# Kernel tuning notes

Hardware: AMD Instinct MI355X
Metric: run time of the kernel (lower is better)

Reference implementation:

```python
import jax, jax.numpy as jnp
import numpy as np
import math

B, S, D, H = 4, 2048, 1024, 16
DH = D // H  # per-head dim = 64
MASK_VAL = -1000000.0


def setup_inputs() -> dict:
    key = jax.random.key(0)
    ks = jax.random.split(key, 9)
    queries = jax.random.normal(ks[0], (B, S, D), dtype=jnp.float32)
    keys = jax.random.normal(ks[1], (B, S, D), dtype=jnp.float32)
    values = jax.random.normal(ks[2], (B, S, D), dtype=jnp.float32)
    valid_lens = jax.random.randint(ks[3], (B,), 0, S, dtype=jnp.int32)
    scale = 1.0 / math.sqrt(D)
    Wq = jax.random.normal(ks[4], (D, D), dtype=jnp.float32) * scale
    Wk = jax.random.normal(ks[5], (D, D), dtype=jnp.float32) * scale
    Wv = jax.random.normal(ks[6], (D, D), dtype=jnp.float32) * scale
    Wo = jax.random.normal(ks[7], (D, D), dtype=jnp.float32) * scale
    return {"queries": queries, "keys": keys, "values": values,
            "valid_lens": valid_lens, "Wq": Wq, "Wk": Wk, "Wv": Wv, "Wo": Wo}


def _split_heads(x):  # [B,S,D] -> [B,H,S,DH]
    b, s, _ = x.shape
    return x.reshape(b, s, H, DH).transpose(0, 2, 1, 3)


def reference(queries, keys, values, valid_lens, Wq, Wk, Wv, Wo):
    q = _split_heads(queries @ Wq)  # [B,H,S,DH]
    k = _split_heads(keys @ Wk)
    v = _split_heads(values @ Wv)
    scores = jnp.einsum('bhqd,bhkd->bhqk', q, k) / jnp.sqrt(jnp.float32(DH))
    # mask key positions >= valid_len[b] (sequence_mask with value=-1e6)
    key_pos = jnp.arange(S)  # [S]
    mask = key_pos[None, None, None, :] < valid_lens[:, None, None, None]  # [B,1,1,S]
    scores = jnp.where(mask, scores, MASK_VAL)
    attn = jax.nn.softmax(scores, axis=-1)  # [B,H,S,S] -- the 1GB intermediate
    out = jnp.einsum('bhqk,bhkd->bhqd', attn, v)  # [B,H,S,DH]
    out = out.transpose(0, 2, 1, 3).reshape(B, S, D)  # concat heads
    return out @ Wo
```

## Files before the change

kernel.cpp:

```cpp
#include <hip/hip_runtime.h>

#define BB 4
#define SS 2048
#define DD 1024
#define HH 16
#define DHH 64

typedef _Float16 half8 __attribute__((ext_vector_type(8)));
typedef _Float16 half4v __attribute__((ext_vector_type(4)));
typedef float floatx4 __attribute__((ext_vector_type(4)));

#define GLOBAL_AS __attribute__((address_space(1)))
#define LDS_AS __attribute__((address_space(3)))

__global__ void wt_kernel(const float* __restrict__ w0, const float* __restrict__ w1,
                          const float* __restrict__ w2, const float* __restrict__ w3,
                          _Float16* __restrict__ wt) {
  __shared__ float tile[32][33];
  int z = blockIdx.z;
  const float* w = (z == 0) ? w0 : (z == 1) ? w1 : (z == 2) ? w2 : w3;
  _Float16* dst = wt + (size_t)z * 1024 * 1024;
  int k0 = blockIdx.x * 32, n0 = blockIdx.y * 32;
  int tx = threadIdx.x & 31, ty = threadIdx.x >> 5;
#pragma unroll
  for (int r = ty; r < 32; r += 8) tile[r][tx] = w[(size_t)(k0 + r) * 1024 + n0 + tx];
  __syncthreads();
#pragma unroll
  for (int r = ty; r < 32; r += 8) dst[(size_t)(n0 + r) * 1024 + k0 + tx] = (_Float16)tile[tx][r];
}

__global__ void cvt3_kernel(const float* __restrict__ q, const float* __restrict__ k,
                            const float* __restrict__ v, _Float16* __restrict__ dst) {
  int z = blockIdx.y;
  const float* src = (z == 0) ? q : (z == 1) ? k : v;
  size_t i = ((size_t)blockIdx.x * 256 + threadIdx.x) * 8;
  float4 f0 = *(const float4*)(src + i);
  float4 f1 = *(const float4*)(src + i + 4);
  half8 h = {(_Float16)f0.x, (_Float16)f0.y, (_Float16)f0.z, (_Float16)f0.w,
             (_Float16)f1.x, (_Float16)f1.y, (_Float16)f1.z, (_Float16)f1.w};
  *(half8*)(dst + (size_t)z * 8388608 + i) = h;
}

__global__ __launch_bounds__(256) void qkv_gemm(const _Float16* __restrict__ Acat,
                                                const _Float16* __restrict__ Wt,
                                                _Float16* __restrict__ Qf,
                                                _Float16* __restrict__ Kf,
                                                _Float16* __restrict__ Vt) {
  __shared__ _Float16 lA[128 * 32];
  __shared__ _Float16 lB[128 * 32];
  int tid = threadIdx.x;
  int wave = tid >> 6, lane = tid & 63, quad = lane >> 4, l15 = lane & 15;
  int bn = blockIdx.x, bm = blockIdx.y;
  int proj = bm >> 6;
  int wm = wave >> 1, wn = wave & 1;

  const _Float16* A = Acat + (size_t)bm * 128 * 1024;
  const _Float16* W = Wt + (size_t)proj * 1024 * 1024;

  floatx4 fzero = {0.f, 0.f, 0.f, 0.f};
  floatx4 acc[4][4];
#pragma unroll
  for (int i = 0; i < 4; ++i)
#pragma unroll
    for (int j = 0; j < 4; ++j) acc[i][j] = fzero;

  int g0 = tid, g1 = 256 + tid;
  int row0 = g0 >> 2, gc0 = (g0 & 3) ^ ((row0 >> 1) & 3);
  int row1 = g1 >> 2, gc1 = (g1 & 3) ^ ((row1 >> 1) & 3);
  const _Float16* a0 = A + ((size_t)row0 * 1024 + gc0 * 8);
  const _Float16* a1 = A + ((size_t)row1 * 1024 + gc1 * 8);
  const _Float16* b0 = W + ((size_t)(bn * 128 + row0) * 1024 + gc0 * 8);
  const _Float16* b1 = W + ((size_t)(bn * 128 + row1) * 1024 + gc1 * 8);

  for (int k0 = 0; k0 < 1024; k0 += 32) {
    __builtin_amdgcn_global_load_lds((const GLOBAL_AS void*)(a0 + k0),
                                     (LDS_AS void*)(lA + g0 * 8), 16, 0, 0);
    __builtin_amdgcn_global_load_lds((const GLOBAL_AS void*)(a1 + k0),
                                     (LDS_AS void*)(lA + g1 * 8), 16, 0, 0);
    __builtin_amdgcn_global_load_lds((const GLOBAL_AS void*)(b0 + k0),
                                     (LDS_AS void*)(lB + g0 * 8), 16, 0, 0);
    __builtin_amdgcn_global_load_lds((const GLOBAL_AS void*)(b1 + k0),
                                     (LDS_AS void*)(lB + g1 * 8), 16, 0, 0);
    __syncthreads();

    half8 af[4], bf[4];
#pragma unroll
    for (int i = 0; i < 4; ++i) {
      int row = wm * 64 + i * 16 + l15;
      af[i] = *(const half8*)(lA + (row * 4 + (quad ^ ((row >> 1) & 3))) * 8);
    }
#pragma unroll
    for (int j = 0; j < 4; ++j) {
      int row = wn * 64 + j * 16 + l15;
      bf[j] = *(const half8*)(lB + (row * 4 + (quad ^ ((row >> 1) & 3))) * 8);
    }
#pragma unroll
    for (int i = 0; i < 4; ++i)
#pragma unroll
      for (int j = 0; j < 4; ++j)
        acc[i][j] = __builtin_amdgcn_mfma_f32_16x16x32_f16(af[i], bf[j], acc[i][j], 0, 0, 0);
    __syncthreads();
  }

  int rloc = (bm & 63) * 128;
#pragma unroll
  for (int i = 0; i < 4; ++i) {
#pragma unroll
    for (int j = 0; j < 4; ++j) {
      int rowb = rloc + wm * 64 + i * 16 + quad * 4;
      int col = bn * 128 + wn * 64 + j * 16 + l15;
      if (proj == 0) {
#pragma unroll
        for (int r = 0; r < 4; ++r)
          Qf[(size_t)(rowb + r) * 1024 + col] = (_Float16)(acc[i][j][r] * 0.125f);
      } else if (proj == 1) {
#pragma unroll
        for (int r = 0; r < 4; ++r)
          Kf[(size_t)(rowb + r) * 1024 + col] = (_Float16)acc[i][j][r];
      } else {
        int b = rowb >> 11, s = rowb & 2047;
        half4v pk = {(_Float16)acc[i][j][0], (_Float16)acc[i][j][1],
                     (_Float16)acc[i][j][2], (_Float16)acc[i][j][3]};
        *(half4v*)(Vt + (size_t)(b * 1024 + col) * 2048 + s) = pk;
      }
    }
  }
}

__global__ __launch_bounds__(256) void gemm_out(const _Float16* __restrict__ A,
                                                const _Float16* __restrict__ Wt,
                                                float* __restrict__ C) {
  __shared__ _Float16 lA[128 * 32];
  __shared__ _Float16 lB[128 * 32];
  int tid = threadIdx.x;
  int wave = tid >> 6, lane = tid & 63, quad = lane >> 4, l15 = lane & 15;
  int bn = blockIdx.x, bm = blockIdx.y;
  int wm = wave >> 1, wn = wave & 1;

  floatx4 fzero = {0.f, 0.f, 0.f, 0.f};
  floatx4 acc[4][4];
#pragma unroll
  for (int i = 0; i < 4; ++i)
#pragma unroll
    for (int j = 0; j < 4; ++j) acc[i][j] = fzero;

  int g0 = tid, g1 = 256 + tid;
  int row0 = g0 >> 2, gc0 = (g0 & 3) ^ ((row0 >> 1) & 3);
  int row1 = g1 >> 2, gc1 = (g1 & 3) ^ ((row1 >> 1) & 3);
  const _Float16* a0 = A + ((size_t)(bm * 128 + row0) * 1024 + gc0 * 8);
  const _Float16* a1 = A + ((size_t)(bm * 128 + row1) * 1024 + gc1 * 8);
  const _Float16* b0 = Wt + ((size_t)(bn * 128 + row0) * 1024 + gc0 * 8);
  const _Float16* b1 = Wt + ((size_t)(bn * 128 + row1) * 1024 + gc1 * 8);

  for (int k0 = 0; k0 < 1024; k0 += 32) {
    __builtin_amdgcn_global_load_lds((const GLOBAL_AS void*)(a0 + k0),
                                     (LDS_AS void*)(lA + g0 * 8), 16, 0, 0);
    __builtin_amdgcn_global_load_lds((const GLOBAL_AS void*)(a1 + k0),
                                     (LDS_AS void*)(lA + g1 * 8), 16, 0, 0);
    __builtin_amdgcn_global_load_lds((const GLOBAL_AS void*)(b0 + k0),
                                     (LDS_AS void*)(lB + g0 * 8), 16, 0, 0);
    __builtin_amdgcn_global_load_lds((const GLOBAL_AS void*)(b1 + k0),
                                     (LDS_AS void*)(lB + g1 * 8), 16, 0, 0);
    __syncthreads();

    half8 af[4], bf[4];
#pragma unroll
    for (int i = 0; i < 4; ++i) {
      int row = wm * 64 + i * 16 + l15;
      af[i] = *(const half8*)(lA + (row * 4 + (quad ^ ((row >> 1) & 3))) * 8);
    }
#pragma unroll
    for (int j = 0; j < 4; ++j) {
      int row = wn * 64 + j * 16 + l15;
      bf[j] = *(const half8*)(lB + (row * 4 + (quad ^ ((row >> 1) & 3))) * 8);
    }
#pragma unroll
    for (int i = 0; i < 4; ++i)
#pragma unroll
      for (int j = 0; j < 4; ++j)
        acc[i][j] = __builtin_amdgcn_mfma_f32_16x16x32_f16(af[i], bf[j], acc[i][j], 0, 0, 0);
    __syncthreads();
  }

#pragma unroll
  for (int i = 0; i < 4; ++i)
#pragma unroll
    for (int j = 0; j < 4; ++j) {
      int rowb = bm * 128 + wm * 64 + i * 16 + quad * 4;
      int col = bn * 128 + wn * 64 + j * 16 + l15;
#pragma unroll
      for (int r = 0; r < 4; ++r) C[(size_t)(rowb + r) * 1024 + col] = acc[i][j][r];
    }
}

__global__ __launch_bounds__(256) void attn_kernel(const _Float16* __restrict__ Q,
                                                   const _Float16* __restrict__ K,
                                                   const _Float16* __restrict__ Vt,
                                                   const int* __restrict__ vlens,
                                                   _Float16* __restrict__ O) {
  __shared__ _Float16 lK[64 * 64];
  __shared__ _Float16 lV[64 * 64];
  __shared__ _Float16 lP[4 * 16 * 64];

  int tid = threadIdx.x, wave = tid >> 6, lane = tid & 63, quad = lane >> 4, l15 = lane & 15;
  int bh = blockIdx.y, b = bh >> 4, h = bh & 15;
  int q0 = blockIdx.x * 64;
  int vlen = vlens[b];
  int nch = (vlen == 0) ? (SS / 64) : ((vlen + 63) >> 6);
  float mask_val = (vlen == 0) ? 0.0f : -1.0e6f;

  const _Float16* qb = Q + ((size_t)(b * SS + q0 + wave * 16 + l15) * DD + h * 64 + quad * 8);
  half8 qf0 = *(const half8*)qb;
  half8 qf1 = *(const half8*)(qb + 32);

  float l_part[4] = {0.f, 0.f, 0.f, 0.f};
  floatx4 fzero = {0.f, 0.f, 0.f, 0.f};
  floatx4 o[4];
#pragma unroll
  for (int j = 0; j < 4; ++j) o[j] = fzero;

  for (int kc = 0; kc < nch; ++kc) {
    int kb = kc * 64;
#pragma unroll
    for (int ss = tid; ss < 512; ss += 256) {
      int row = ss >> 3, gc = ss & 7;
      int sidx = (row * 8 + (gc ^ (row & 7))) * 8;
      *(half8*)(lK + sidx) =
          *(const half8*)(K + ((size_t)(b * SS + kb + row) * DD + h * 64 + gc * 8));
      *(half8*)(lV + sidx) =
          *(const half8*)(Vt + ((size_t)(b * DD + h * 64 + row) * SS + kb + gc * 8));
    }
    __syncthreads();

    floatx4 sacc[4];
#pragma unroll
    for (int j = 0; j < 4; ++j) sacc[j] = fzero;
#pragma unroll
    for (int ks = 0; ks < 2; ++ks) {
      half8 qf = ks ? qf1 : qf0;
#pragma unroll
      for (int j = 0; j < 4; ++j) {
        int row = j * 16 + l15, gc = ks * 4 + quad;
        half8 kf = *(const half8*)(lK + (row * 8 + (gc ^ (row & 7))) * 8);
        sacc[j] = __builtin_amdgcn_mfma_f32_16x16x32_f16(qf, kf, sacc[j], 0, 0, 0);
      }
    }

    bool clean = (kb + 64 <= vlen);
#pragma unroll
    for (int j = 0; j < 4; ++j) {
      int key = kb + j * 16 + l15;
      bool valid = clean | (key < vlen);
#pragma unroll
      for (int r = 0; r < 4; ++r) {
        float s = valid ? sacc[j][r] : mask_val;
        float p = __expf(s);
        l_part[r] += p;
        int row = quad * 4 + r, col = j * 16 + l15;
        int gc = col >> 3, off = col & 7;
        lP[wave * 1024 + row * 64 + (gc ^ (row & 7)) * 8 + off] = (_Float16)p;
      }
    }

#pragma unroll
    for (int ks = 0; ks < 2; ++ks) {
      int gc = ks * 4 + quad;
      half8 pf = *(const half8*)(lP + wave * 1024 + l15 * 64 + (gc ^ (l15 & 7)) * 8);
#pragma unroll
      for (int j = 0; j < 4; ++j) {
        int row = j * 16 + l15;
        half8 vf = *(const half8*)(lV + (row * 8 + (gc ^ (row & 7))) * 8);
        o[j] = __builtin_amdgcn_mfma_f32_16x16x32_f16(pf, vf, o[j], 0, 0, 0);
      }
    }
    __syncthreads();
  }

  float inv_l[4];
#pragma unroll
  for (int r = 0; r < 4; ++r) {
    float l = l_part[r];
#pragma unroll
    for (int off = 1; off < 16; off <<= 1) l += __shfl_xor(l, off);
    inv_l[r] = 1.0f / l;
  }
#pragma unroll
  for (int j = 0; j < 4; ++j) {
    int col = h * 64 + j * 16 + l15;
#pragma unroll
    for (int r = 0; r < 4; ++r) {
      int qrow = q0 + wave * 16 + quad * 4 + r;
      O[(size_t)(b * SS + qrow) * DD + col] = (_Float16)(o[j][r] * inv_l[r]);
    }
  }
}

extern "C" void kernel_launch(void* const* d_in, const int* in_sizes, int n_in,
                              void* d_out, int out_size, void* d_ws, size_t ws_size,
                              hipStream_t stream) {
  const float* q = (const float*)d_in[0];
  const float* k = (const float*)d_in[1];
  const float* v = (const float*)d_in[2];
  const int* vl = (const int*)d_in[3];
  const float* wq = (const float*)d_in[4];
  const float* wk = (const float*)d_in[5];
  const float* wv = (const float*)d_in[6];
  const float* wo = (const float*)d_in[7];

  char* ws = (char*)d_ws;
  _Float16* Wt = (_Float16*)ws;
  _Float16* Acat = (_Float16*)(ws + (8u << 20));
  _Float16* Qf = (_Float16*)(ws + (56u << 20));
  _Float16* Kf = (_Float16*)(ws + (72u << 20));
  _Float16* Vt = (_Float16*)(ws + (88u << 20));
  _Float16* Of = Acat;

  dim3 blk(256);

  wt_kernel<<<dim3(32, 32, 4), blk, 0, stream>>>(wq, wk, wv, wo, Wt);
  cvt3_kernel<<<dim3(4096, 3), blk, 0, stream>>>(q, k, v, Acat);
  qkv_gemm<<<dim3(8, 192), blk, 0, stream>>>(Acat, Wt, Qf, Kf, Vt);
  attn_kernel<<<dim3(32, 64), blk, 0, stream>>>(Qf, Kf, Vt, vl, Of);
  gemm_out<<<dim3(8, 64), blk, 0, stream>>>(Of, Wt + (3u << 20), (float*)d_out);
}
```

Measured before the change: 340.0 us.

## Merge prep kernels, fold Q scale into weights, split-K output GEMM with atomics

```diff
diff --git a/kernel.cpp b/kernel.cpp
--- a/kernel.cpp
+++ b/kernel.cpp
@@ -13,32 +13,43 @@
 #define GLOBAL_AS __attribute__((address_space(1)))
 #define LDS_AS __attribute__((address_space(3)))
 
-__global__ void wt_kernel(const float* __restrict__ w0, const float* __restrict__ w1,
-                          const float* __restrict__ w2, const float* __restrict__ w3,
-                          _Float16* __restrict__ wt) {
-  __shared__ float tile[32][33];
-  int z = blockIdx.z;
-  const float* w = (z == 0) ? w0 : (z == 1) ? w1 : (z == 2) ? w2 : w3;
-  _Float16* dst = wt + (size_t)z * 1024 * 1024;
-  int k0 = blockIdx.x * 32, n0 = blockIdx.y * 32;
-  int tx = threadIdx.x & 31, ty = threadIdx.x >> 5;
-#pragma unroll
-  for (int r = ty; r < 32; r += 8) tile[r][tx] = w[(size_t)(k0 + r) * 1024 + n0 + tx];
-  __syncthreads();
-#pragma unroll
-  for (int r = ty; r < 32; r += 8) dst[(size_t)(n0 + r) * 1024 + k0 + tx] = (_Float16)tile[tx][r];
-}
-
-__global__ void cvt3_kernel(const float* __restrict__ q, const float* __restrict__ k,
-                            const float* __restrict__ v, _Float16* __restrict__ dst) {
-  int z = blockIdx.y;
-  const float* src = (z == 0) ? q : (z == 1) ? k : v;
-  size_t i = ((size_t)blockIdx.x * 256 + threadIdx.x) * 8;
-  float4 f0 = *(const float4*)(src + i);
-  float4 f1 = *(const float4*)(src + i + 4);
-  half8 h = {(_Float16)f0.x, (_Float16)f0.y, (_Float16)f0.z, (_Float16)f0.w,
-             (_Float16)f1.x, (_Float16)f1.y, (_Float16)f1.z, (_Float16)f1.w};
-  *(half8*)(dst + (size_t)z * 8388608 + i) = h;
+__global__ void prep_kernel(const float* __restrict__ q, const float* __restrict__ k,
+                            const float* __restrict__ v, const float* __restrict__ wq,
+                            const float* __restrict__ wk, const float* __restrict__ wv,
+                            const float* __restrict__ wo, _Float16* __restrict__ wt,
+                            _Float16* __restrict__ acat, float* __restrict__ dout) {
+  int bx = blockIdx.x;
+  if (bx < 4096) {
+    __shared__ float tile[32][33];
+    int z = bx >> 10, rem = bx & 1023;
+    const float* w = (z == 0) ? wq : (z == 1) ? wk : (z == 2) ? wv : wo;
+    float scale = (z == 0) ? 0.125f : 1.0f;
+    _Float16* dst = wt + (size_t)z * 1048576;
+    int k0 = (rem >> 5) * 32, n0 = (rem & 31) * 32;
+    int tx = threadIdx.x & 31, ty = threadIdx.x >> 5;
+#pragma unroll
+    for (int r = ty; r < 32; r += 8) tile[r][tx] = w[(size_t)(k0 + r) * 1024 + n0 + tx];
+    __syncthreads();
+#pragma unroll
+    for (int r = ty; r < 32; r += 8)
+      dst[(size_t)(n0 + r) * 1024 + k0 + tx] = (_Float16)(tile[tx][r] * scale);
+  } else if (bx < 16384) {
+    int idx = bx - 4096;
+    int z = idx >> 12, xx = idx & 4095;
+    const float* src = (z == 0) ? q : (z == 1) ? k : v;
+    size_t i = ((size_t)xx * 256 + threadIdx.x) * 8;
+    float4 f0 = *(const float4*)(src + i);
+    float4 f1 = *(const float4*)(src + i + 4);
+    half8 h = {(_Float16)f0.x, (_Float16)f0.y, (_Float16)f0.z, (_Float16)f0.w,
+               (_Float16)f1.x, (_Float16)f1.y, (_Float16)f1.z, (_Float16)f1.w};
+    *(half8*)(acat + (size_t)z * 8388608 + i) = h;
+  } else {
+    int idx = bx - 16384;
+    size_t i = ((size_t)idx * 256 + threadIdx.x) * 8;
+    float4 zz = {0.f, 0.f, 0.f, 0.f};
+    *(float4*)(dout + i) = zz;
+    *(float4*)(dout + i + 4) = zz;
+  }
 }
 
 __global__ __launch_bounds__(256) void qkv_gemm(const _Float16* __restrict__ Acat,
@@ -109,14 +120,11 @@
     for (int j = 0; j < 4; ++j) {
       int rowb = rloc + wm * 64 + i * 16 + quad * 4;
       int col = bn * 128 + wn * 64 + j * 16 + l15;
-      if (proj == 0) {
+      if (proj < 2) {
+        _Float16* dst = (proj == 0) ? Qf : Kf;
 #pragma unroll
         for (int r = 0; r < 4; ++r)
-          Qf[(size_t)(rowb + r) * 1024 + col] = (_Float16)(acc[i][j][r] * 0.125f);
-      } else if (proj == 1) {
-#pragma unroll
-        for (int r = 0; r < 4; ++r)
-          Kf[(size_t)(rowb + r) * 1024 + col] = (_Float16)acc[i][j][r];
+          dst[(size_t)(rowb + r) * 1024 + col] = (_Float16)acc[i][j][r];
       } else {
         int b = rowb >> 11, s = rowb & 2047;
         half4v pk = {(_Float16)acc[i][j][0], (_Float16)acc[i][j][1],
@@ -134,7 +142,7 @@
   __shared__ _Float16 lB[128 * 32];
   int tid = threadIdx.x;
   int wave = tid >> 6, lane = tid & 63, quad = lane >> 4, l15 = lane & 15;
-  int bn = blockIdx.x, bm = blockIdx.y;
+  int bn = blockIdx.x, bm = blockIdx.y, kz = blockIdx.z;
   int wm = wave >> 1, wn = wave & 1;
 
   floatx4 fzero = {0.f, 0.f, 0.f, 0.f};
@@ -152,7 +160,8 @@
   const _Float16* b0 = Wt + ((size_t)(bn * 128 + row0) * 1024 + gc0 * 8);
   const _Float16* b1 = Wt + ((size_t)(bn * 128 + row1) * 1024 + gc1 * 8);
 
-  for (int k0 = 0; k0 < 1024; k0 += 32) {
+  int kbeg = kz * 512, kend = kbeg + 512;
+  for (int k0 = kbeg; k0 < kend; k0 += 32) {
     __builtin_amdgcn_global_load_lds((const GLOBAL_AS void*)(a0 + k0),
                                      (LDS_AS void*)(lA + g0 * 8), 16, 0, 0);
     __builtin_amdgcn_global_load_lds((const GLOBAL_AS void*)(a1 + k0),
@@ -189,7 +198,8 @@
       int rowb = bm * 128 + wm * 64 + i * 16 + quad * 4;
       int col = bn * 128 + wn * 64 + j * 16 + l15;
 #pragma unroll
-      for (int r = 0; r < 4; ++r) C[(size_t)(rowb + r) * 1024 + col] = acc[i][j][r];
+      for (int r = 0; r < 4; ++r)
+        atomicAdd(&C[(size_t)(rowb + r) * 1024 + col], acc[i][j][r]);
     }
 }
 
@@ -317,9 +327,9 @@
 
   dim3 blk(256);
 
-  wt_kernel<<<dim3(32, 32, 4), blk, 0, stream>>>(wq, wk, wv, wo, Wt);
-  cvt3_kernel<<<dim3(4096, 3), blk, 0, stream>>>(q, k, v, Acat);
+  prep_kernel<<<dim3(20480), blk, 0, stream>>>(q, k, v, wq, wk, wv, wo, Wt, Acat,
+                                               (float*)d_out);
   qkv_gemm<<<dim3(8, 192), blk, 0, stream>>>(Acat, Wt, Qf, Kf, Vt);
   attn_kernel<<<dim3(32, 64), blk, 0, stream>>>(Qf, Kf, Vt, vl, Of);
-  gemm_out<<<dim3(8, 64), blk, 0, stream>>>(Of, Wt + (3u << 20), (float*)d_out);
-}
+  gemm_out<<<dim3(8, 64, 2), blk, 0, stream>>>(Of, Wt + 3 * 1048576, (float*)d_out);
+}
```

Result: slower. 384.5 us (+13.1%).
